# Kernel tuning notes

Measured on AMD Instinct MI355X. Metric: run time of the kernel, lower is better.

Reference implementation:

```python
import jax, jax.numpy as jnp
import numpy as np


def _retain(o1, others, W, bias):
    # o1: (b, s, h); others: (b, 4, s, h); W: (h, h); bias: (1,)
    q = o1 @ W                                        # (b, s, h)
    scores = jnp.einsum('bih,bkjh->bijk', q, others) + bias[0]  # (b, s1, s2, 4)
    w = jax.nn.softmax(scores, axis=-1)               # softmax over the 4 options
    # weight[:, :, :, k] @ option_k summed over k
    return jnp.einsum('bijk,bkjh->bih', w, others)


def setup_inputs() -> dict:
    key = jax.random.key(0)
    ks = jax.random.split(key, 7)
    b, s, h = 32, 256, 1024
    opts = {f'option{i+1}': jax.random.normal(ks[i], (b, s, h), dtype=jnp.float32)
            for i in range(5)}
    W = 0.02 * jax.random.normal(ks[5], (h, h), dtype=jnp.float32)
    bias = 0.02 * jax.random.normal(ks[6], (1,), dtype=jnp.float32)
    return {**opts, 'W': W, 'bias': bias}


def reference(option1, option2, option3, option4, option5, W, bias):
    opts = [option1, option2, option3, option4, option5]
    total = None
    for i in range(5):
        others = jnp.stack([opts[j] for j in range(5) if j != i], axis=1)  # (b,4,s,h)
        r = _retain(opts[i], others, W, bias)
        total = r if total is None else total + r
    return total / 2.0
```

## Files before the change

kernel.cpp:

```cpp
#include <hip/hip_runtime.h>
#include <hip/hip_bf16.h>
#include <stdint.h>


#define BB 32
#define SS 256
#define HH 1024

typedef __attribute__((ext_vector_type(4))) float f32x4;
typedef __attribute__((ext_vector_type(8))) __bf16 bf16x8;
typedef __attribute__((ext_vector_type(4))) __bf16 bf16x4;

__device__ constexpr int PAIR(int i, int n) { return i * 4 + (n > i ? n - 1 : n); }

__device__ __forceinline__ void gload_lds16(const void* g, void* l) {
  __builtin_amdgcn_global_load_lds((const __attribute__((address_space(1))) void*)g,
                                   (__attribute__((address_space(3))) void*)l, 16, 0, 0);
}

__global__ void canary(float* out, float v) { out[0] = v; }

__global__ __launch_bounds__(256) void cast_all(
    const float* p0, const float* p1, const float* p2, const float* p3, const float* p4,
    __bf16* __restrict__ dst)
{
  int m = blockIdx.x >> 12;
  long off = ((long)(blockIdx.x & 4095) * 256 + threadIdx.x) * 8;
  const float* src = m == 0 ? p0 : m == 1 ? p1 : m == 2 ? p2 : m == 3 ? p3 : p4;
  float4 v0 = *(const float4*)(src + off);
  float4 v1 = *(const float4*)(src + off + 4);
  bf16x8 h;
  h[0] = (__bf16)v0.x; h[1] = (__bf16)v0.y; h[2] = (__bf16)v0.z; h[3] = (__bf16)v0.w;
  h[4] = (__bf16)v1.x; h[5] = (__bf16)v1.y; h[6] = (__bf16)v1.z; h[7] = (__bf16)v1.w;
  *(bf16x8*)(dst + (long)m * BB * SS * HH + off) = h;
}

__global__ __launch_bounds__(256) void cast_trW(const float* __restrict__ src,
                                                __bf16* __restrict__ dstT)
{
  __shared__ __bf16 tile[64][72];
  int ct = blockIdx.x & 15, rt = blockIdx.x >> 4;
  const float* s = src + (long)(rt * 64) * 1024 + ct * 64;
  int t = threadIdx.x;
#pragma unroll
  for (int p = 0; p < 4; p++) {
    int c = t + p * 256;
    int row = c >> 4, c4 = c & 15;
    float4 v = *(const float4*)(s + (long)row * 1024 + c4 * 4);
    bf16x4 h;
    h[0] = (__bf16)v.x; h[1] = (__bf16)v.y; h[2] = (__bf16)v.z; h[3] = (__bf16)v.w;
    *(bf16x4*)&tile[row][c4 * 4] = h;
  }
  __syncthreads();
#pragma unroll
  for (int p = 0; p < 4; p++) {
    int c = t + p * 256;
    int hr = c >> 4, s4 = c & 15;
    bf16x4 h;
    h[0] = tile[s4 * 4 + 0][hr];
    h[1] = tile[s4 * 4 + 1][hr];
    h[2] = tile[s4 * 4 + 2][hr];
    h[3] = tile[s4 * 4 + 3][hr];
    *(bf16x4*)(dstT + (long)(ct * 64 + hr) * 1024 + rt * 64 + s4 * 4) = h;
  }
}

__global__ __launch_bounds__(256) void qgemm_b16(
    const __bf16* __restrict__ A, const __bf16* __restrict__ Bt, __bf16* __restrict__ C)
{
  __shared__ __align__(16) __bf16 smA[128][32];
  __shared__ __align__(16) __bf16 smB[128][32];
  int lin = blockIdx.x;
  int xcd = lin & 7, idx = lin >> 3;
  int rt = xcd * 40 + (idx >> 3), ct = idx & 7;
  int t = threadIdx.x, l = t & 63, w = t >> 6;
  int wm = w >> 1, wn = w & 1;
  f32x4 acc[4][4] = {};
  for (int k0 = 0; k0 < 1024; k0 += 32) {
#pragma unroll
    for (int p = 0; p < 2; p++) {
      int c = t + p * 256;
      int row = c >> 2, half = c & 3;
      gload_lds16(A + (long)(rt * 128 + row) * 1024 + k0 + half * 8,
                  (char*)smA + ((c >> 6) << 10));
      gload_lds16(Bt + (long)(ct * 128 + row) * 1024 + k0 + half * 8,
                  (char*)smB + ((c >> 6) << 10));
    }
    __syncthreads();
    bf16x8 af[4], bfr[4];
    int sl = l >> 4, lr = l & 15;
#pragma unroll
    for (int i = 0; i < 4; i++) {
      af[i]  = *(const bf16x8*)&smA[wm * 64 + i * 16 + lr][sl * 8];
      bfr[i] = *(const bf16x8*)&smB[wn * 64 + i * 16 + lr][sl * 8];
    }
#pragma unroll
    for (int i = 0; i < 4; i++)
#pragma unroll
      for (int j = 0; j < 4; j++)
        acc[i][j] = __builtin_amdgcn_mfma_f32_16x16x32_bf16(af[i], bfr[j], acc[i][j], 0, 0, 0);
    __syncthreads();
  }
#pragma unroll
  for (int i = 0; i < 4; i++) {
    long mrow = (long)rt * 128 + wm * 64 + i * 16 + ((l >> 4) << 2);
#pragma unroll
    for (int j = 0; j < 4; j++) {
      int n = ct * 128 + wn * 64 + j * 16 + (l & 15);
#pragma unroll
      for (int r = 0; r < 4; r++)
        C[(mrow + r) * 1024 + n] = (__bf16)acc[i][j][r];
    }
  }
}

__global__ __launch_bounds__(256, 2) void gram_b16(
    const __bf16* __restrict__ Q, const __bf16* __restrict__ O, __bf16* __restrict__ V)
{
  __shared__ __align__(16) char ldsb[3 * 20480];
  int bid = blockIdx.x;
  int xcd = bid & 7, idx = bid >> 3;
  int b = xcd * 4 + (idx >> 6);
  int rem = idx & 63;
  int s1t = rem >> 3, s2t = rem & 7;
  int t = threadIdx.x, l = t & 63, w = t >> 6;
  int pr = w >> 1, pc = w & 1;
  f32x4 acc[20] = {};

  long qrow0 = (long)b * SS + s1t * 32;
  long orow0 = (long)b * SS + s2t * 32;
  int slog = (l & 3) ^ ((l >> 3) & 3);
  const char* gp0; const char* gp1; const char* gp2; const char* gp3; const char* gp4;
#define GP_INIT(GP, P)                                                                \
  {                                                                                   \
    int g = 4 * (P) + w;                                                              \
    int isQ = g < 10;                                                                 \
    int gg = isQ ? g : g - 10;                                                        \
    long row = (long)(gg >> 1) * (BB * SS) + (isQ ? qrow0 : orow0) + (g & 1) * 16 +   \
               (l >> 2);                                                              \
    GP = (const char*)((isQ ? Q : O) + row * HH + slog * 8);                          \
  }
  GP_INIT(gp0, 0) GP_INIT(gp1, 1) GP_INIT(gp2, 2) GP_INIT(gp3, 3) GP_INIT(gp4, 4)
#undef GP_INIT
  int g0 = w, g1 = 4 + w, g2 = 8 + w, g3 = 12 + w, g4 = 16 + w;

#define STAGE(BB_)                                                      \
  {                                                                     \
    char* base = ldsb + (BB_) * 20480;                                  \
    gload_lds16(gp0, base + g0 * 1024); gp0 += 64;                      \
    gload_lds16(gp1, base + g1 * 1024); gp1 += 64;                      \
    gload_lds16(gp2, base + g2 * 1024); gp2 += 64;                      \
    gload_lds16(gp3, base + g3 * 1024); gp3 += 64;                      \
    gload_lds16(gp4, base + g4 * 1024); gp4 += 64;                      \
  }

  int lr = l & 15, sl = l >> 4;
  int swz = (sl ^ ((lr >> 1) & 3)) * 16;
  int qoff = (pr * 16 + lr) * 64 + swz;
  int ooff = 10240 + (pc * 16 + lr) * 64 + swz;

#define COMPUTE(BB_)                                                                   \
  {                                                                                    \
    const char* base = ldsb + (BB_) * 20480;                                           \
    bf16x8 qf[5], of[5];                                                               \
    _Pragma("unroll") for (int m = 0; m < 5; m++) {                                    \
      qf[m] = *(const bf16x8*)(base + m * 2048 + qoff);                                \
      of[m] = *(const bf16x8*)(base + m * 2048 + ooff);                                \
    }                                                                                  \
    __builtin_amdgcn_s_setprio(1);                                                     \
    _Pragma("unroll") for (int i = 0; i < 5; i++) {                                    \
      _Pragma("unroll") for (int n = 0; n < 5; n++) {                                  \
        if (n != i)                                                                    \
          acc[PAIR(i, n)] =                                                            \
              __builtin_amdgcn_mfma_f32_16x16x32_bf16(qf[i], of[n], acc[PAIR(i, n)],   \
                                                      0, 0, 0);                        \
      }                                                                                \
    }                                                                                  \
    __builtin_amdgcn_s_setprio(0);                                                     \
  }

#define STEP(CUR, STG)                                          \
  asm volatile("s_waitcnt vmcnt(5)" ::: "memory");              \
  __builtin_amdgcn_s_barrier();                                 \
  STAGE(STG);                                                   \
  COMPUTE(CUR);

  STAGE(0)
  STAGE(1)
  for (int it = 0; it < 10; it++) {
    STEP(0, 2)
    STEP(1, 0)
    STEP(2, 1)
  }
  asm volatile("s_waitcnt vmcnt(5)" ::: "memory");
  __builtin_amdgcn_s_barrier();
  COMPUTE(0)
  asm volatile("s_waitcnt vmcnt(0)" ::: "memory");
  __builtin_amdgcn_s_barrier();
  COMPUTE(1)
#undef STEP
#undef COMPUTE
#undef STAGE

  int s1g = s1t * 32 + pr * 16 + ((l >> 4) << 2);
  int s2g = s2t * 32 + pc * 16 + (l & 15);
#pragma unroll
  for (int r = 0; r < 4; r++) {
    float vacc[5] = {0.f, 0.f, 0.f, 0.f, 0.f};
#pragma unroll
    for (int i = 0; i < 5; i++) {
      float gg[5];
      float mx = -3.0e38f;
#pragma unroll
      for (int n = 0; n < 5; n++)
        if (n != i) { gg[n] = acc[PAIR(i, n)][r]; mx = fmaxf(mx, gg[n]); }
      float ee[5], ssum = 0.f;
#pragma unroll
      for (int n = 0; n < 5; n++)
        if (n != i) { ee[n] = __expf(gg[n] - mx); ssum += ee[n]; }
      float inv = 1.0f / ssum;
#pragma unroll
      for (int n = 0; n < 5; n++)
        if (n != i) vacc[n] += ee[n] * inv;
    }
#pragma unroll
    for (int n = 0; n < 5; n++)
      V[((long)(n * 32 + b) * 256 + s1g + r) * 256 + s2g] = (__bf16)vacc[n];
  }
}

__global__ __launch_bounds__(256) void pvgemm(
    const __bf16* __restrict__ Vb, const __bf16* __restrict__ Obf, float* __restrict__ out)
{
  __shared__ __bf16 smA[128][40];
  __shared__ __bf16 smB[128][40];
  int bid = blockIdx.x;
  int b = bid >> 4, s1t = (bid >> 3) & 1, ht = bid & 7;
  int t = threadIdx.x, l = t & 63, w = t >> 6;
  int wm = w >> 1, wn = w & 1;
  f32x4 acc[4][4] = {};
#pragma unroll
  for (int n = 0; n < 5; n++) {
    const __bf16* On = Obf + (long)n * BB * SS * HH;
    for (int st2 = 0; st2 < 8; st2++) {
      int s20 = st2 * 32;
#pragma unroll
      for (int p = 0; p < 2; p++) {
        int c = t + p * 256;
        int row = c >> 2, sl = c & 3;
        *(bf16x8*)&smA[row][sl * 8] =
            *(const bf16x8*)(Vb + (long)(n * BB + b) * SS * SS + (long)(s1t * 128 + row) * SS +
                             s20 + sl * 8);
      }
      {
        int h4 = (t & 31) * 4, s2q = (t >> 5) * 4;
        const __bf16* src = On + ((long)b * 256 + s20 + s2q) * 1024 + ht * 128 + h4;
        bf16x4 v0 = *(const bf16x4*)(src);
        bf16x4 v1 = *(const bf16x4*)(src + 1024);
        bf16x4 v2 = *(const bf16x4*)(src + 2048);
        bf16x4 v3 = *(const bf16x4*)(src + 3072);
        bf16x4 c0, c1, c2, c3;
        c0[0] = v0[0]; c0[1] = v1[0]; c0[2] = v2[0]; c0[3] = v3[0];
        c1[0] = v0[1]; c1[1] = v1[1]; c1[2] = v2[1]; c1[3] = v3[1];
        c2[0] = v0[2]; c2[1] = v1[2]; c2[2] = v2[2]; c2[3] = v3[2];
        c3[0] = v0[3]; c3[1] = v1[3]; c3[2] = v2[3]; c3[3] = v3[3];
        *(bf16x4*)&smB[h4 + 0][s2q] = c0;
        *(bf16x4*)&smB[h4 + 1][s2q] = c1;
        *(bf16x4*)&smB[h4 + 2][s2q] = c2;
        *(bf16x4*)&smB[h4 + 3][s2q] = c3;
      }
      __syncthreads();
      bf16x8 af[4], bfr[4];
      int sl = l >> 4, lr = l & 15;
#pragma unroll
      for (int i = 0; i < 4; i++) {
        af[i]  = *(const bf16x8*)&smA[wm * 64 + i * 16 + lr][sl * 8];
        bfr[i] = *(const bf16x8*)&smB[wn * 64 + i * 16 + lr][sl * 8];
      }
#pragma unroll
      for (int i = 0; i < 4; i++)
#pragma unroll
        for (int j = 0; j < 4; j++)
          acc[i][j] = __builtin_amdgcn_mfma_f32_16x16x32_bf16(af[i], bfr[j], acc[i][j], 0, 0, 0);
      __syncthreads();
    }
  }
#pragma unroll
  for (int i = 0; i < 4; i++) {
    int m = s1t * 128 + wm * 64 + i * 16 + ((l >> 4) << 2);
#pragma unroll
    for (int j = 0; j < 4; j++) {
      int n = ht * 128 + wn * 64 + j * 16 + (l & 15);
#pragma unroll
      for (int r = 0; r < 4; r++)
        out[(long)(b * SS + m + r) * HH + n] = 0.5f * acc[i][j][r];
    }
  }
}

extern "C" void kernel_launch(void* const* d_in, const int* in_sizes, int n_in,
                              void* d_out, int out_size, void* d_ws, size_t ws_size,
                              hipStream_t stream)
{
  const size_t SZ_W = (size_t)HH * HH * 2;
  const size_t SZ_Q = (size_t)5 * BB * SS * HH * 2;
  const size_t SZ_V = (size_t)5 * BB * SS * SS * 2;
  const size_t SZ_O = (size_t)5 * BB * SS * HH * 2;
  const size_t NEED = SZ_W + SZ_Q + SZ_V + SZ_O;
  if (ws_size < NEED) {
    canary<<<1, 1, 0, stream>>>((float*)d_out, (float)(ws_size >> 20));
    return;
  }
  char* ws = (char*)d_ws;
  __bf16* Wt  = (__bf16*)ws;
  __bf16* Qb  = (__bf16*)(ws + SZ_W);
  __bf16* Vb  = (__bf16*)(ws + SZ_W + SZ_Q);
  __bf16* Obf = (__bf16*)(ws + SZ_W + SZ_Q + SZ_V);
  const float* o0 = (const float*)d_in[0];
  const float* o1 = (const float*)d_in[1];
  const float* o2 = (const float*)d_in[2];
  const float* o3 = (const float*)d_in[3];
  const float* o4 = (const float*)d_in[4];

  cast_trW<<<256, 256, 0, stream>>>((const float*)d_in[5], Wt);
  cast_all<<<5 * 4096, 256, 0, stream>>>(o0, o1, o2, o3, o4, Obf);
  qgemm_b16<<<2560, 256, 0, stream>>>(Obf, Wt, Qb);
  gram_b16<<<2048, 256, 0, stream>>>(Qb, Obf, Vb);
  pvgemm<<<512, 256, 0, stream>>>(Vb, Obf, (float*)d_out);
}
```

Measured before the change: 303.1 us.

## Triple-buffer qgemm LDS loads with swizzled layout and async prefetch

Rewrites the Q-projection GEMM main loop as a three-stage LDS ring. Global-to-LDS loads for future k-tiles are issued while MFMAs run on the current tile, synchronised with vmcnt waits and a single barrier per step. It also XOR-swizzles the LDS column placement to reduce bank conflicts on fragment reads, raises wave priority around the MFMA block, and requests 3 blocks per CU. The cost is triple the LDS footprint and hand-managed wait counts that must stay consistent with the number of loads issued per stage.

```diff
diff --git a/kernel.cpp b/kernel.cpp
--- a/kernel.cpp
+++ b/kernel.cpp
@@ -65,42 +65,82 @@
   }
 }
 
-__global__ __launch_bounds__(256) void qgemm_b16(
+__global__ __launch_bounds__(256, 3) void qgemm_b16(
     const __bf16* __restrict__ A, const __bf16* __restrict__ Bt, __bf16* __restrict__ C)
 {
-  __shared__ __align__(16) __bf16 smA[128][32];
-  __shared__ __align__(16) __bf16 smB[128][32];
+  __shared__ __align__(16) char ldsb[3 * 16384];
   int lin = blockIdx.x;
   int xcd = lin & 7, idx = lin >> 3;
   int rt = xcd * 40 + (idx >> 3), ct = idx & 7;
   int t = threadIdx.x, l = t & 63, w = t >> 6;
   int wm = w >> 1, wn = w & 1;
   f32x4 acc[4][4] = {};
-  for (int k0 = 0; k0 < 1024; k0 += 32) {
-#pragma unroll
-    for (int p = 0; p < 2; p++) {
-      int c = t + p * 256;
-      int row = c >> 2, half = c & 3;
-      gload_lds16(A + (long)(rt * 128 + row) * 1024 + k0 + half * 8,
-                  (char*)smA + ((c >> 6) << 10));
-      gload_lds16(Bt + (long)(ct * 128 + row) * 1024 + k0 + half * 8,
-                  (char*)smB + ((c >> 6) << 10));
-    }
-    __syncthreads();
-    bf16x8 af[4], bfr[4];
-    int sl = l >> 4, lr = l & 15;
-#pragma unroll
-    for (int i = 0; i < 4; i++) {
-      af[i]  = *(const bf16x8*)&smA[wm * 64 + i * 16 + lr][sl * 8];
-      bfr[i] = *(const bf16x8*)&smB[wn * 64 + i * 16 + lr][sl * 8];
-    }
-#pragma unroll
-    for (int i = 0; i < 4; i++)
-#pragma unroll
-      for (int j = 0; j < 4; j++)
-        acc[i][j] = __builtin_amdgcn_mfma_f32_16x16x32_bf16(af[i], bfr[j], acc[i][j], 0, 0, 0);
-    __syncthreads();
-  }
+
+  const char *gA0, *gA1, *gB0, *gB1;
+  {
+    int c0 = t, c1 = t + 256;
+    int r0 = c0 >> 2, h0 = (c0 & 3) ^ ((c0 >> 3) & 3);
+    int r1 = c1 >> 2, h1 = (c1 & 3) ^ ((c1 >> 3) & 3);
+    gA0 = (const char*)(A + (long)(rt * 128 + r0) * 1024 + h0 * 8);
+    gA1 = (const char*)(A + (long)(rt * 128 + r1) * 1024 + h1 * 8);
+    gB0 = (const char*)(Bt + (long)(ct * 128 + r0) * 1024 + h0 * 8);
+    gB1 = (const char*)(Bt + (long)(ct * 128 + r1) * 1024 + h1 * 8);
+  }
+  int dst0 = w * 1024, dst1 = (w + 4) * 1024;
+
+#define STAGE(BUF)                                                \
+  {                                                               \
+    char* base = ldsb + (BUF) * 16384;                            \
+    gload_lds16(gA0, base + dst0); gA0 += 64;                     \
+    gload_lds16(gA1, base + dst1); gA1 += 64;                     \
+    gload_lds16(gB0, base + 8192 + dst0); gB0 += 64;              \
+    gload_lds16(gB1, base + 8192 + dst1); gB1 += 64;              \
+  }
+
+  int lr = l & 15, sl = l >> 4;
+  int swz = (sl ^ ((lr >> 1) & 3)) * 16;
+  int aoff = (wm * 64 + lr) * 64 + swz;
+  int boff = 8192 + (wn * 64 + lr) * 64 + swz;
+
+#define COMPUTE(BUF)                                                                   \
+  {                                                                                    \
+    const char* base = ldsb + (BUF) * 16384;                                           \
+    bf16x8 af[4], bfr[4];                                                              \
+    _Pragma("unroll") for (int i = 0; i < 4; i++) {                                    \
+      af[i]  = *(const bf16x8*)(base + aoff + i * 1024);                               \
+      bfr[i] = *(const bf16x8*)(base + boff + i * 1024);                               \
+    }                                                                                  \
+    __builtin_amdgcn_s_setprio(1);                                                     \
+    _Pragma("unroll") for (int i = 0; i < 4; i++)                                      \
+      _Pragma("unroll") for (int j = 0; j < 4; j++)                                    \
+        acc[i][j] = __builtin_amdgcn_mfma_f32_16x16x32_bf16(af[i], bfr[j],             \
+                                                            acc[i][j], 0, 0, 0);       \
+    __builtin_amdgcn_s_setprio(0);                                                     \
+  }
+
+#define STEP(CUR, STG)                                          \
+  asm volatile("s_waitcnt vmcnt(4)" ::: "memory");              \
+  __builtin_amdgcn_s_barrier();                                 \
+  STAGE(STG);                                                   \
+  COMPUTE(CUR);
+
+  STAGE(0)
+  STAGE(1)
+  for (int it = 0; it < 10; it++) {
+    STEP(0, 2)
+    STEP(1, 0)
+    STEP(2, 1)
+  }
+  asm volatile("s_waitcnt vmcnt(4)" ::: "memory");
+  __builtin_amdgcn_s_barrier();
+  COMPUTE(0)
+  asm volatile("s_waitcnt vmcnt(0)" ::: "memory");
+  __builtin_amdgcn_s_barrier();
+  COMPUTE(1)
+#undef STEP
+#undef COMPUTE
+#undef STAGE
+
 #pragma unroll
   for (int i = 0; i < 4; i++) {
     long mrow = (long)rt * 128 + wm * 64 + i * 16 + ((l >> 4) << 2);
```

New measurement: 294.9 us. -2.7%, faster.

## Rewrite Q GEMM as 256x256 double-buffered tile with swizzled LDS

Applied to the files above, without the earlier changes.

Replaces the 128x128, K=32 single-buffered Q projection GEMM with a 256x256 tile, K=64 step, 512-thread kernel. Global-to-LDS loads for the next K slice are interleaved with MFMAs on the current buffer, and the LDS layout uses an XOR swizzle to avoid bank conflicts. MFMA sections run at raised wave priority. The goal is to hide global load latency and raise arithmetic intensity, at the cost of 128KB of LDS per block and a large accumulator register footprint, which may limit occupancy.

```diff
diff --git a/kernel.cpp b/kernel.cpp
--- a/kernel.cpp
+++ b/kernel.cpp
@@ -65,48 +65,96 @@
   }
 }
 
-__global__ __launch_bounds__(256) void qgemm_b16(
+__global__ __launch_bounds__(512, 2) void qgemm256(
     const __bf16* __restrict__ A, const __bf16* __restrict__ Bt, __bf16* __restrict__ C)
 {
-  __shared__ __align__(16) __bf16 smA[128][32];
-  __shared__ __align__(16) __bf16 smB[128][32];
+  __shared__ __align__(16) char ldsb[2 * 65536];
   int lin = blockIdx.x;
   int xcd = lin & 7, idx = lin >> 3;
-  int rt = xcd * 40 + (idx >> 3), ct = idx & 7;
+  int rt = xcd * 20 + (idx >> 2), ct = idx & 3;
   int t = threadIdx.x, l = t & 63, w = t >> 6;
-  int wm = w >> 1, wn = w & 1;
-  f32x4 acc[4][4] = {};
-  for (int k0 = 0; k0 < 1024; k0 += 32) {
-#pragma unroll
-    for (int p = 0; p < 2; p++) {
-      int c = t + p * 256;
-      int row = c >> 2, half = c & 3;
-      gload_lds16(A + (long)(rt * 128 + row) * 1024 + k0 + half * 8,
-                  (char*)smA + ((c >> 6) << 10));
-      gload_lds16(Bt + (long)(ct * 128 + row) * 1024 + k0 + half * 8,
-                  (char*)smB + ((c >> 6) << 10));
-    }
-    __syncthreads();
-    bf16x8 af[4], bfr[4];
-    int sl = l >> 4, lr = l & 15;
-#pragma unroll
-    for (int i = 0; i < 4; i++) {
-      af[i]  = *(const bf16x8*)&smA[wm * 64 + i * 16 + lr][sl * 8];
-      bfr[i] = *(const bf16x8*)&smB[wn * 64 + i * 16 + lr][sl * 8];
-    }
-#pragma unroll
-    for (int i = 0; i < 4; i++)
-#pragma unroll
-      for (int j = 0; j < 4; j++)
-        acc[i][j] = __builtin_amdgcn_mfma_f32_16x16x32_bf16(af[i], bfr[j], acc[i][j], 0, 0, 0);
-    __syncthreads();
-  }
-#pragma unroll
-  for (int i = 0; i < 4; i++) {
-    long mrow = (long)rt * 128 + wm * 64 + i * 16 + ((l >> 4) << 2);
+  int wr = w >> 2, wc = w & 3;
+  f32x4 acc[8][4] = {};
+
+  const char* gp[8];
+  int dstp[8];
+#pragma unroll
+  for (int p = 0; p < 8; p++) {
+    int c = t + 512 * (p & 3);
+    int row = c >> 3;
+    int sg = (c & 7) ^ (row & 7);
+    if (p < 4) {
+      gp[p] = (const char*)(A + (long)(rt * 256 + row) * 1024 + sg * 8);
+      dstp[p] = w * 1024 + (p & 3) * 8192;
+    } else {
+      gp[p] = (const char*)(Bt + (long)(ct * 256 + row) * 1024 + sg * 8);
+      dstp[p] = 32768 + w * 1024 + (p & 3) * 8192;
+    }
+  }
+
+  int lr = l & 15, sl = l >> 4;
+  int sx0 = (sl ^ (lr & 7)) * 16;
+  int sx1 = ((4 | sl) ^ (lr & 7)) * 16;
+  int arow = (wr * 128 + lr) * 128;
+  int brow = 32768 + (wc * 64 + lr) * 128;
+
+#define TILE(CUR, DOSTAGE)                                                             \
+  {                                                                                    \
+    const char* base = ldsb + (CUR) * 65536;                                           \
+    char* sbase = ldsb + ((CUR) ^ 1) * 65536;                                          \
+    bf16x8 bfr[4][2], af[2][2];                                                        \
+    _Pragma("unroll") for (int j = 0; j < 4; j++) {                                    \
+      bfr[j][0] = *(const bf16x8*)(base + brow + j * 2048 + sx0);                      \
+      bfr[j][1] = *(const bf16x8*)(base + brow + j * 2048 + sx1);                      \
+    }                                                                                  \
+    _Pragma("unroll") for (int ph = 0; ph < 4; ph++) {                                 \
+      if (DOSTAGE) {                                                                   \
+        gload_lds16(gp[ph], sbase + dstp[ph]);                                         \
+        gload_lds16(gp[ph + 4], sbase + dstp[ph + 4]);                                 \
+      }                                                                                \
+      _Pragma("unroll") for (int ii = 0; ii < 2; ii++) {                               \
+        int i = ph * 2 + ii;                                                           \
+        af[ii][0] = *(const bf16x8*)(base + arow + i * 2048 + sx0);                    \
+        af[ii][1] = *(const bf16x8*)(base + arow + i * 2048 + sx1);                    \
+      }                                                                                \
+      __builtin_amdgcn_s_setprio(1);                                                   \
+      _Pragma("unroll") for (int ii = 0; ii < 2; ii++)                                 \
+        _Pragma("unroll") for (int j = 0; j < 4; j++) {                                \
+          acc[ph * 2 + ii][j] = __builtin_amdgcn_mfma_f32_16x16x32_bf16(               \
+              af[ii][0], bfr[j][0], acc[ph * 2 + ii][j], 0, 0, 0);                     \
+          acc[ph * 2 + ii][j] = __builtin_amdgcn_mfma_f32_16x16x32_bf16(               \
+              af[ii][1], bfr[j][1], acc[ph * 2 + ii][j], 0, 0, 0);                     \
+        }                                                                              \
+      __builtin_amdgcn_s_setprio(0);                                                   \
+    }                                                                                  \
+    if (DOSTAGE) {                                                                     \
+      _Pragma("unroll") for (int p = 0; p < 8; p++) gp[p] += 128;                      \
+    }                                                                                  \
+  }
+
+  {
+#pragma unroll
+    for (int p = 0; p < 8; p++) {
+      gload_lds16(gp[p], ldsb + dstp[p]);
+      gp[p] += 128;
+    }
+  }
+  asm volatile("s_waitcnt vmcnt(0)" ::: "memory");
+  __builtin_amdgcn_s_barrier();
+  for (int tt = 0; tt < 15; tt++) {
+    TILE(tt & 1, 1)
+    asm volatile("s_waitcnt vmcnt(0)" ::: "memory");
+    __builtin_amdgcn_s_barrier();
+  }
+  TILE(1, 0)
+#undef TILE
+
+#pragma unroll
+  for (int i = 0; i < 8; i++) {
+    long mrow = (long)rt * 256 + wr * 128 + i * 16 + (sl << 2);
 #pragma unroll
     for (int j = 0; j < 4; j++) {
-      int n = ct * 128 + wn * 64 + j * 16 + (l & 15);
+      int n = ct * 256 + wc * 64 + j * 16 + lr;
 #pragma unroll
       for (int r = 0; r < 4; r++)
         C[(mrow + r) * 1024 + n] = (__bf16)acc[i][j][r];
@@ -324,7 +372,7 @@
 
   cast_trW<<<256, 256, 0, stream>>>((const float*)d_in[5], Wt);
   cast_all<<<5 * 4096, 256, 0, stream>>>(o0, o1, o2, o3, o4, Obf);
-  qgemm_b16<<<2560, 256, 0, stream>>>(Obf, Wt, Qb);
+  qgemm256<<<640, 512, 0, stream>>>(Obf, Wt, Qb);
   gram_b16<<<2048, 256, 0, stream>>>(Qb, Obf, Vb);
   pvgemm<<<512, 256, 0, stream>>>(Vb, Obf, (float*)d_out);
 }
```

New measurement: 279.9 us. 7.7% less time.
